# Kernel tuning notes

Hardware: AMD Instinct MI355X
Metric: run time of the kernel (lower is better)

## Reference

```python
import jax, jax.numpy as jnp
import numpy as np

B, K, D = 8, 1024, 512
H, DQ, DV = 8, 64, 64


def setup_inputs() -> dict:
    key = jax.random.key(0)
    ks = jax.random.split(key, 11)
    s = 0.02  # param init scale
    return {
        "query": jax.random.normal(ks[0], (B, K, D), jnp.float32),
        "key": jax.random.normal(ks[1], (B, K, D), jnp.float32),
        "value": jax.random.normal(ks[2], (B, K, D), jnp.float32),
        "Wq": jax.random.normal(ks[3], (D, H * DQ), jnp.float32) * s,
        "bq": jax.random.normal(ks[4], (H * DQ,), jnp.float32) * s,
        "Wk": jax.random.normal(ks[5], (D, H * DQ), jnp.float32) * s,
        "bk": jax.random.normal(ks[6], (H * DQ,), jnp.float32) * s,
        "Wv": jax.random.normal(ks[7], (D, H * DV), jnp.float32) * s,
        "bv": jax.random.normal(ks[8], (H * DV,), jnp.float32) * s,
        "Wo": jax.random.normal(ks[9], (H * DV, D), jnp.float32) * s,
        "bo": jax.random.normal(ks[10], (D,), jnp.float32) * s,
    }


def reference(query, key, value, Wq, bq, Wk, bk, Wv, bv, Wo, bo):
    b, k, _ = query.shape
    # Linear projections, split into heads: chunk(h, dim=-1) + cat(dim=0)
    # is equivalent to reshape (b, k, h, d) with head on a separate axis.
    q = (query @ Wq + bq).reshape(b, k, H, DQ)  # b k h dq
    kk = (key @ Wk + bk).reshape(b, k, H, DQ)   # b k h dq
    v = (value @ Wv + bv).reshape(b, k, H, DV)  # b k h dv
    # NOTE: original scales by sqrt(K) (sequence length), not sqrt(dq).
    scale = 1.0 / jnp.sqrt(jnp.asarray(k, q.dtype))
    scores = jnp.einsum("bqhd,bkhd->bhqk", q, kk) * scale
    attn = jax.nn.softmax(scores, axis=-1)
    ctx = jnp.einsum("bhqk,bkhd->bqhd", attn, v).reshape(b, k, H * DV)
    return ctx @ Wo + bo
```

## Files before the change

kernel.cpp:

```cpp
#include <hip/hip_runtime.h>
#include <hip/hip_bf16.h>

#define DEVI __device__ __forceinline__

typedef __attribute__((ext_vector_type(4))) float f32x4;
typedef __attribute__((ext_vector_type(8))) short bf16x8;

static constexpr int BB  = 8;
static constexpr int SEQ = 1024;
static constexpr int DIM = 512;
static constexpr int NH  = 8;
static constexpr int HD  = 64;
static constexpr int M   = BB * SEQ;


DEVI unsigned short f2bf(float x) {
  unsigned int u = __builtin_bit_cast(unsigned int, x);
  u += 0x7fffu + ((u >> 16) & 1u);
  return (unsigned short)(u >> 16);
}

DEVI float fexp2(float x) {
#if __has_builtin(__builtin_amdgcn_exp2f)
  return __builtin_amdgcn_exp2f(x);
#else
  float r; asm("v_exp_f32 %0, %1" : "=v"(r) : "v"(x)); return r;
#endif
}

DEVI void gload_lds16(const unsigned short* g, unsigned short* l) {
  __builtin_amdgcn_global_load_lds(
      (const __attribute__((address_space(1))) void*)g,
      (__attribute__((address_space(3))) void*)l, 16, 0, 0);
}


__global__ __launch_bounds__(256) void cvt3_kernel(const float* __restrict__ a,
                                                   const float* __restrict__ b,
                                                   const float* __restrict__ c,
                                                   unsigned short* __restrict__ oa,
                                                   unsigned short* __restrict__ ob,
                                                   unsigned short* __restrict__ oc) {
  const float* in = (blockIdx.y == 0) ? a : ((blockIdx.y == 1) ? b : c);
  unsigned short* out = (blockIdx.y == 0) ? oa : ((blockIdx.y == 1) ? ob : oc);
  int i = (blockIdx.x * 256 + threadIdx.x) * 4;
  float4 v = *reinterpret_cast<const float4*>(in + i);
  ushort4 o;
  o.x = f2bf(v.x); o.y = f2bf(v.y); o.z = f2bf(v.z); o.w = f2bf(v.w);
  *reinterpret_cast<ushort4*>(out + i) = o;
}


__global__ __launch_bounds__(256) void cvt_t4_kernel(const float* __restrict__ w0,
                                                     const float* __restrict__ w1,
                                                     const float* __restrict__ w2,
                                                     const float* __restrict__ w3,
                                                     unsigned short* __restrict__ o0,
                                                     unsigned short* __restrict__ o1,
                                                     unsigned short* __restrict__ o2,
                                                     unsigned short* __restrict__ o3) {
  const float* in = (blockIdx.z == 0) ? w0 : ((blockIdx.z == 1) ? w1 : ((blockIdx.z == 2) ? w2 : w3));
  unsigned short* out = (blockIdx.z == 0) ? o0 : ((blockIdx.z == 1) ? o1 : ((blockIdx.z == 2) ? o2 : o3));
  __shared__ float tile[32][33];
  int n0 = blockIdx.x * 32, k0 = blockIdx.y * 32;
  int tx = threadIdx.x & 31, ty = threadIdx.x >> 5;
#pragma unroll
  for (int r = 0; r < 32; r += 8)
    tile[ty + r][tx] = in[(size_t)(k0 + ty + r) * DIM + n0 + tx];
  __syncthreads();
#pragma unroll
  for (int r = 0; r < 32; r += 8)
    out[(size_t)(n0 + ty + r) * DIM + k0 + tx] = f2bf(tile[tx][ty + r]);
}


__global__ __launch_bounds__(256) void gemm_proj(const unsigned short* __restrict__ Aq,
                                                 const unsigned short* __restrict__ Ak,
                                                 const unsigned short* __restrict__ Av,
                                                 const unsigned short* __restrict__ WqT,
                                                 const unsigned short* __restrict__ WkT,
                                                 const unsigned short* __restrict__ WvT,
                                                 const float* __restrict__ bq,
                                                 const float* __restrict__ bk,
                                                 const float* __restrict__ bv,
                                                 unsigned short* __restrict__ qb,
                                                 unsigned short* __restrict__ kb,
                                                 unsigned short* __restrict__ vT,
                                                 float qscale) {
  __shared__ unsigned short smem[24576];
  unsigned short* lA = smem;
  unsigned short* lB = smem + 12288;

  const int z = blockIdx.z;
  const unsigned short* A = (z == 0) ? Aq : ((z == 1) ? Ak : Av);
  const unsigned short* Bt = (z == 0) ? WqT : ((z == 1) ? WkT : WvT);
  const float* bias = (z == 0) ? bq : ((z == 1) ? bk : bv);
  const float gs = (z == 0) ? qscale : 1.0f;

  const int tid = threadIdx.x;
  const int lane = tid & 63, wave = tid >> 6;
  const int wr = wave >> 1, wc = wave & 1;
  const int row0 = blockIdx.x * 128, col0 = blockIdx.y * 128;
  const int lr = lane & 15, lg = lane >> 4;

  f32x4 acc[4][4] = {};

  const int s0a = wave * 64;
  const int sA = s0a + lane, rA = sA >> 2, koA = (sA & 3) * 8;
  const int s0b = 256 + wave * 64;
  const int sB = s0b + lane, rB = sB >> 2, koB = (sB & 3) * 8;

#define GEMM_STAGE(buf, k0)                                                              \
  do {                                                                                   \
    gload_lds16(A + (size_t)(row0 + rA) * DIM + (k0) + koA, &lA[(buf)*4096 + s0a * 8]);  \
    gload_lds16(Bt + (size_t)(col0 + rA) * DIM + (k0) + koA, &lB[(buf)*4096 + s0a * 8]); \
    gload_lds16(A + (size_t)(row0 + rB) * DIM + (k0) + koB, &lA[(buf)*4096 + s0b * 8]);  \
    gload_lds16(Bt + (size_t)(col0 + rB) * DIM + (k0) + koB, &lB[(buf)*4096 + s0b * 8]); \
  } while (0)

#define GEMM_STEP(cur, VMC)                                                              \
  do {                                                                                   \
    asm volatile("s_waitcnt vmcnt(" #VMC ")" ::: "memory");                              \
    __builtin_amdgcn_s_barrier();                                                        \
    bf16x8 af[4], bfr[4];                                                                \
    _Pragma("unroll")                                                                    \
    for (int m = 0; m < 4; ++m)                                                          \
      af[m] = *reinterpret_cast<const bf16x8*>(&lA[(cur)*4096 + (wr * 64 + m * 16 + lr) * 32 + lg * 8]); \
    _Pragma("unroll")                                                                    \
    for (int n = 0; n < 4; ++n)                                                          \
      bfr[n] = *reinterpret_cast<const bf16x8*>(&lB[(cur)*4096 + (wc * 64 + n * 16 + lr) * 32 + lg * 8]); \
    __builtin_amdgcn_s_setprio(1);                                                       \
    _Pragma("unroll")                                                                    \
    for (int m = 0; m < 4; ++m)                                                          \
      _Pragma("unroll")                                                                  \
      for (int n = 0; n < 4; ++n)                                                        \
        acc[m][n] = __builtin_amdgcn_mfma_f32_16x16x32_bf16(af[m], bfr[n], acc[m][n], 0, 0, 0); \
    __builtin_amdgcn_s_setprio(0);                                                       \
    asm volatile("" ::: "memory");                                                       \
    __builtin_amdgcn_s_barrier();                                                        \
  } while (0)

  constexpr int NT = DIM / 32;
  GEMM_STAGE(0, 0);
  GEMM_STAGE(1, 32);
  for (int t = 0; t < NT - 2; ++t) {
    GEMM_STAGE((t + 2) % 3, (t + 2) * 32);
    GEMM_STEP(t % 3, 8);
  }
  GEMM_STEP((NT - 2) % 3, 4);
  GEMM_STEP((NT - 1) % 3, 0);
#undef GEMM_STAGE
#undef GEMM_STEP

  if (z < 2) {
    unsigned short* C = (z == 0) ? qb : kb;
#pragma unroll
    for (int m = 0; m < 4; ++m) {
#pragma unroll
      for (int n = 0; n < 4; ++n) {
        int col = col0 + wc * 64 + n * 16 + lr;
        int r0 = row0 + wr * 64 + m * 16 + lg * 4;
        float bvv = bias[col];
#pragma unroll
        for (int j = 0; j < 4; ++j)
          C[(size_t)(r0 + j) * DIM + col] = f2bf((acc[m][n][j] + bvv) * gs);
      }
    }
  } else {
    unsigned short* ldsT = smem;
    __syncthreads();
#pragma unroll
    for (int m = 0; m < 4; ++m) {
#pragma unroll
      for (int n = 0; n < 4; ++n) {
        const int col = wc * 64 + n * 16 + lr;
        const int r0l = wr * 64 + m * 16 + lg * 4;
        const float bvv = bias[col0 + col];
        ushort4 pk;
        pk.x = f2bf(acc[m][n][0] + bvv);
        pk.y = f2bf(acc[m][n][1] + bvv);
        pk.z = f2bf(acc[m][n][2] + bvv);
        pk.w = f2bf(acc[m][n][3] + bvv);
        *reinterpret_cast<ushort4*>(&ldsT[col * 136 + r0l]) = pk;
      }
    }
    __syncthreads();
    const int b = row0 >> 10, s_loc0 = row0 & 1023;
#pragma unroll
    for (int it = 0; it < 8; ++it) {
      int idx = it * 256 + tid;
      int c = idx >> 4, s8 = idx & 15;
      bf16x8 v = *reinterpret_cast<const bf16x8*>(&ldsT[c * 136 + s8 * 8]);
      *reinterpret_cast<bf16x8*>(
          vT + ((size_t)(b * DIM) + col0 + c) * SEQ + s_loc0 + s8 * 8) = v;
    }
  }
}


__global__ __launch_bounds__(256) void gemm_out(const unsigned short* __restrict__ A,
                                                const unsigned short* __restrict__ Bt,
                                                const float* __restrict__ bias,
                                                float* __restrict__ C) {
  __shared__ unsigned short lA[3][128 * 32];
  __shared__ unsigned short lB[3][128 * 32];
  const int tid = threadIdx.x;
  const int lane = tid & 63, wave = tid >> 6;
  const int wr = wave >> 1, wc = wave & 1;
  const int row0 = blockIdx.x * 128, col0 = blockIdx.y * 128;
  const int lr = lane & 15, lg = lane >> 4;

  f32x4 acc[4][4] = {};

  const int s0a = wave * 64;
  const int sA = s0a + lane, rA = sA >> 2, koA = (sA & 3) * 8;
  const int s0b = 256 + wave * 64;
  const int sB = s0b + lane, rB = sB >> 2, koB = (sB & 3) * 8;

#define GEMM_STAGE(buf, k0)                                                        \
  do {                                                                             \
    gload_lds16(A + (size_t)(row0 + rA) * DIM + (k0) + koA, &lA[buf][s0a * 8]);    \
    gload_lds16(Bt + (size_t)(col0 + rA) * DIM + (k0) + koA, &lB[buf][s0a * 8]);   \
    gload_lds16(A + (size_t)(row0 + rB) * DIM + (k0) + koB, &lA[buf][s0b * 8]);    \
    gload_lds16(Bt + (size_t)(col0 + rB) * DIM + (k0) + koB, &lB[buf][s0b * 8]);   \
  } while (0)

#define GEMM_STEP(cur, VMC)                                                        \
  do {                                                                             \
    asm volatile("s_waitcnt vmcnt(" #VMC ")" ::: "memory");                        \
    __builtin_amdgcn_s_barrier();                                                  \
    bf16x8 af[4], bfr[4];                                                          \
    _Pragma("unroll")                                                              \
    for (int m = 0; m < 4; ++m)                                                    \
      af[m] = *reinterpret_cast<const bf16x8*>(&lA[cur][(wr * 64 + m * 16 + lr) * 32 + lg * 8]); \
    _Pragma("unroll")                                                              \
    for (int n = 0; n < 4; ++n)                                                    \
      bfr[n] = *reinterpret_cast<const bf16x8*>(&lB[cur][(wc * 64 + n * 16 + lr) * 32 + lg * 8]); \
    __builtin_amdgcn_s_setprio(1);                                                 \
    _Pragma("unroll")                                                              \
    for (int m = 0; m < 4; ++m)                                                    \
      _Pragma("unroll")                                                            \
      for (int n = 0; n < 4; ++n)                                                  \
        acc[m][n] = __builtin_amdgcn_mfma_f32_16x16x32_bf16(af[m], bfr[n], acc[m][n], 0, 0, 0); \
    __builtin_amdgcn_s_setprio(0);                                                 \
    asm volatile("" ::: "memory");                                                 \
    __builtin_amdgcn_s_barrier();                                                  \
  } while (0)

  constexpr int NT = DIM / 32;
  GEMM_STAGE(0, 0);
  GEMM_STAGE(1, 32);
  for (int t = 0; t < NT - 2; ++t) {
    GEMM_STAGE((t + 2) % 3, (t + 2) * 32);
    GEMM_STEP((t % 3), 8);
  }
  GEMM_STEP(((NT - 2) % 3), 4);
  GEMM_STEP(((NT - 1) % 3), 0);
#undef GEMM_STAGE
#undef GEMM_STEP

#pragma unroll
  for (int m = 0; m < 4; ++m) {
#pragma unroll
    for (int n = 0; n < 4; ++n) {
      int col = col0 + wc * 64 + n * 16 + lr;
      int r0 = row0 + wr * 64 + m * 16 + lg * 4;
      float bv = bias[col];
#pragma unroll
      for (int j = 0; j < 4; ++j)
        C[(size_t)(r0 + j) * DIM + col] = acc[m][n][j] + bv;
    }
  }
}


__global__ __launch_bounds__(512) void attn_kernel(const unsigned short* __restrict__ qb,
                                                   const unsigned short* __restrict__ kb,
                                                   const unsigned short* __restrict__ vT,
                                                   unsigned short* __restrict__ ctx) {
  __shared__ unsigned short lK[2][64 * 64];
  __shared__ unsigned short lV[2][64 * 64];
  __shared__ unsigned short Pl[8][16 * 72];

  const int b = blockIdx.z, h = blockIdx.y;
  const int tid = threadIdx.x, lane = tid & 63, wave = tid >> 6;
  const int lr = lane & 15, lg = lane >> 4;
  const int q0 = blockIdx.x * 128 + wave * 16;

  const int sr = tid >> 3, sc = (tid & 7) ^ (sr & 7);
  const unsigned short* Kbase = kb + ((size_t)b * SEQ) * DIM + (size_t)h * HD;
  const unsigned short* Vbase = vT + (size_t)(b * NH + h) * HD * SEQ;

  bf16x8 qf0, qf1;
  {
    const unsigned short* qrow = qb + ((size_t)(b * SEQ) + q0 + lr) * DIM + h * HD;
    qf0 = *reinterpret_cast<const bf16x8*>(qrow + lg * 8);
    qf1 = *reinterpret_cast<const bf16x8*>(qrow + 32 + lg * 8);
  }

  float l_r[4] = {0.f, 0.f, 0.f, 0.f};
  f32x4 o_acc[4];
#pragma unroll
  for (int n = 0; n < 4; ++n) o_acc[n] = f32x4{0.f, 0.f, 0.f, 0.f};

  unsigned short* pw = Pl[wave];

#define ATT_STAGE(buf, nk)                                                          \
  do {                                                                              \
    gload_lds16(Kbase + (size_t)((nk) + sr) * DIM + sc * 8, &lK[buf][(wave * 64) * 8]); \
    gload_lds16(Vbase + (size_t)sr * SEQ + (nk) + sc * 8, &lV[buf][(wave * 64) * 8]);   \
  } while (0)

#define ATT_COMPUTE(cur)                                                            \
  do {                                                                              \
    f32x4 st[4];                                                                    \
    __builtin_amdgcn_s_setprio(1);                                                  \
    _Pragma("unroll")                                                               \
    for (int kt = 0; kt < 4; ++kt) {                                                \
      const int row = kt * 16 + lr;                                                 \
      const char* rbase = (const char*)&lK[cur][0] + row * 128;                     \
      const int sw = (row & 7) << 4;                                                \
      bf16x8 kf0 = *reinterpret_cast<const bf16x8*>(rbase + ((lg * 16) ^ sw));      \
      bf16x8 kf1 = *reinterpret_cast<const bf16x8*>(rbase + ((64 + lg * 16) ^ sw)); \
      f32x4 a = {};                                                                 \
      a = __builtin_amdgcn_mfma_f32_16x16x32_bf16(qf0, kf0, a, 0, 0, 0);            \
      a = __builtin_amdgcn_mfma_f32_16x16x32_bf16(qf1, kf1, a, 0, 0, 0);            \
      st[kt] = a;                                                                   \
    }                                                                               \
    __builtin_amdgcn_s_setprio(0);                                                  \
    _Pragma("unroll")                                                               \
    for (int j = 0; j < 4; ++j) {                                                   \
      float p0 = fexp2(st[0][j]);                                                   \
      float p1 = fexp2(st[1][j]);                                                   \
      float p2 = fexp2(st[2][j]);                                                   \
      float p3 = fexp2(st[3][j]);                                                   \
      l_r[j] += (p0 + p1) + (p2 + p3);                                              \
      const int qrow = (lg * 4 + j) * 72;                                           \
      pw[qrow + lr] = f2bf(p0);                                                     \
      pw[qrow + 16 + lr] = f2bf(p1);                                                \
      pw[qrow + 32 + lr] = f2bf(p2);                                                \
      pw[qrow + 48 + lr] = f2bf(p3);                                                \
    }                                                                               \
    _Pragma("unroll")                                                               \
    for (int c = 0; c < 2; ++c) {                                                   \
      bf16x8 pf = *reinterpret_cast<const bf16x8*>((const char*)pw + lr * 144 + c * 64 + lg * 16); \
      __builtin_amdgcn_s_setprio(1);                                                \
      _Pragma("unroll")                                                             \
      for (int n = 0; n < 4; ++n) {                                                 \
        const int row = n * 16 + lr;                                                \
        bf16x8 vf = *reinterpret_cast<const bf16x8*>(                               \
            (const char*)&lV[cur][0] + row * 128 + ((c * 64 + lg * 16) ^ ((row & 7) << 4))); \
        o_acc[n] = __builtin_amdgcn_mfma_f32_16x16x32_bf16(pf, vf, o_acc[n], 0, 0, 0); \
      }                                                                             \
      __builtin_amdgcn_s_setprio(0);                                                \
    }                                                                               \
  } while (0)

  constexpr int NTT = SEQ / 64;
  ATT_STAGE(0, 0);
  for (int t = 0; t < NTT - 1; ++t) {
    const int cur = t & 1;
    ATT_STAGE(cur ^ 1, (t + 1) * 64);
    asm volatile("s_waitcnt vmcnt(2)" ::: "memory");
    __builtin_amdgcn_s_barrier();
    ATT_COMPUTE(cur);
    asm volatile("" ::: "memory");
    __builtin_amdgcn_s_barrier();
  }
  asm volatile("s_waitcnt vmcnt(0)" ::: "memory");
  __builtin_amdgcn_s_barrier();
  ATT_COMPUTE((NTT - 1) & 1);
#undef ATT_STAGE
#undef ATT_COMPUTE

  float invl[4];
#pragma unroll
  for (int j = 0; j < 4; ++j) {
    float l = l_r[j];
#pragma unroll
    for (int msk = 1; msk < 16; msk <<= 1) l += __shfl_xor(l, msk);
    invl[j] = 1.f / l;
  }
#pragma unroll
  for (int n = 0; n < 4; ++n)
#pragma unroll
    for (int j = 0; j < 4; ++j)
      pw[(lg * 4 + j) * 72 + n * 16 + lr] = f2bf(o_acc[n][j] * invl[j]);

#pragma unroll
  for (int it = 0; it < 2; ++it) {
    int idx = it * 64 + lane;
    int r = idx >> 3, cc = idx & 7;
    bf16x8 v = *reinterpret_cast<const bf16x8*>((const char*)pw + r * 144 + cc * 16);
    *reinterpret_cast<bf16x8*>(ctx + ((size_t)(b * SEQ) + q0 + r) * DIM + h * HD + cc * 8) = v;
  }
}


extern "C" void kernel_launch(void* const* d_in, const int* in_sizes, int n_in,
                              void* d_out, int out_size, void* d_ws, size_t ws_size,
                              hipStream_t stream) {
  const float* query = (const float*)d_in[0];
  const float* key_  = (const float*)d_in[1];
  const float* value = (const float*)d_in[2];
  const float* Wq = (const float*)d_in[3];
  const float* bq = (const float*)d_in[4];
  const float* Wk = (const float*)d_in[5];
  const float* bk = (const float*)d_in[6];
  const float* Wv = (const float*)d_in[7];
  const float* bv = (const float*)d_in[8];
  const float* Wo = (const float*)d_in[9];
  const float* bo = (const float*)d_in[10];
  float* out = (float*)d_out;

  unsigned short* ws = (unsigned short*)d_ws;
  const size_t NM = (size_t)M * DIM;
  const size_t NW = (size_t)DIM * DIM;
  unsigned short* xq   = ws;
  unsigned short* xk   = xq + NM;
  unsigned short* xv   = xk + NM;
  unsigned short* qb   = xv + NM;
  unsigned short* kbuf = qb + NM;
  unsigned short* vTb  = kbuf + NM;
  unsigned short* ctx  = vTb + NM;
  unsigned short* Wqt  = ctx + NM;
  unsigned short* Wkt  = Wqt + NW;
  unsigned short* Wvt  = Wkt + NW;
  unsigned short* Wot  = Wvt + NW;

  cvt3_kernel<<<dim3((int)(NM / 1024), 3), 256, 0, stream>>>(query, key_, value, xq, xk, xv);
  cvt_t4_kernel<<<dim3(16, 16, 4), 256, 0, stream>>>(Wq, Wk, Wv, Wo, Wqt, Wkt, Wvt, Wot);

  const float qscale = 0.03125f * 1.4426950408889634f;
  gemm_proj<<<dim3(M / 128, DIM / 128, 3), 256, 0, stream>>>(
      xq, xk, xv, Wqt, Wkt, Wvt, bq, bk, bv, qb, kbuf, vTb, qscale);

  attn_kernel<<<dim3(SEQ / 128, NH, BB), 512, 0, stream>>>(qb, kbuf, vTb, ctx);

  gemm_out<<<dim3(M / 128, DIM / 128), 256, 0, stream>>>(ctx, Wot, bo, out);
}
```

Baseline: 81.41 us.

## Fuse fp32-to-bf16 activation conversion into projection GEMM loads

```diff
diff --git a/kernel.cpp b/kernel.cpp
--- a/kernel.cpp
+++ b/kernel.cpp
@@ -34,20 +34,25 @@
       (__attribute__((address_space(3))) void*)l, 16, 0, 0);
 }
 
-
-__global__ __launch_bounds__(256) void cvt3_kernel(const float* __restrict__ a,
-                                                   const float* __restrict__ b,
-                                                   const float* __restrict__ c,
-                                                   unsigned short* __restrict__ oa,
-                                                   unsigned short* __restrict__ ob,
-                                                   unsigned short* __restrict__ oc) {
-  const float* in = (blockIdx.y == 0) ? a : ((blockIdx.y == 1) ? b : c);
-  unsigned short* out = (blockIdx.y == 0) ? oa : ((blockIdx.y == 1) ? ob : oc);
-  int i = (blockIdx.x * 256 + threadIdx.x) * 4;
-  float4 v = *reinterpret_cast<const float4*>(in + i);
-  ushort4 o;
-  o.x = f2bf(v.x); o.y = f2bf(v.y); o.z = f2bf(v.z); o.w = f2bf(v.w);
-  *reinterpret_cast<ushort4*>(out + i) = o;
+DEVI void gload_lds16f(const float* g, float* l) {
+  __builtin_amdgcn_global_load_lds(
+      (const __attribute__((address_space(1))) void*)g,
+      (__attribute__((address_space(3))) void*)l, 16, 0, 0);
+}
+
+DEVI unsigned int cvtpk(float lo, float hi) {
+  unsigned int r;
+  asm("v_cvt_pk_bf16_f32 %0, %1, %2" : "=v"(r) : "v"(lo), "v"(hi));
+  return r;
+}
+
+DEVI bf16x8 cvt8pk(float4 a, float4 b) {
+  union { unsigned int u[4]; bf16x8 v; } r;
+  r.u[0] = cvtpk(a.x, a.y);
+  r.u[1] = cvtpk(a.z, a.w);
+  r.u[2] = cvtpk(b.x, b.y);
+  r.u[3] = cvtpk(b.z, b.w);
+  return r.v;
 }
 
 
@@ -74,9 +79,9 @@
 }
 
 
-__global__ __launch_bounds__(256) void gemm_proj(const unsigned short* __restrict__ Aq,
-                                                 const unsigned short* __restrict__ Ak,
-                                                 const unsigned short* __restrict__ Av,
+__global__ __launch_bounds__(256) void gemm_proj(const float* __restrict__ Aq,
+                                                 const float* __restrict__ Ak,
+                                                 const float* __restrict__ Av,
                                                  const unsigned short* __restrict__ WqT,
                                                  const unsigned short* __restrict__ WkT,
                                                  const unsigned short* __restrict__ WvT,
@@ -87,12 +92,12 @@
                                                  unsigned short* __restrict__ kb,
                                                  unsigned short* __restrict__ vT,
                                                  float qscale) {
-  __shared__ unsigned short smem[24576];
-  unsigned short* lA = smem;
-  unsigned short* lB = smem + 12288;
+  __shared__ __align__(16) char smem[49152];
+  float* lAf = (float*)smem;
+  unsigned short* lB = (unsigned short*)(smem + 32768);
 
   const int z = blockIdx.z;
-  const unsigned short* A = (z == 0) ? Aq : ((z == 1) ? Ak : Av);
+  const float* A32 = (z == 0) ? Aq : ((z == 1) ? Ak : Av);
   const unsigned short* Bt = (z == 0) ? WqT : ((z == 1) ? WkT : WvT);
   const float* bias = (z == 0) ? bq : ((z == 1) ? bk : bv);
   const float gs = (z == 0) ? qscale : 1.0f;
@@ -105,27 +110,42 @@
 
   f32x4 acc[4][4] = {};
 
+  int arow[4], acsrc[4];
+#pragma unroll
+  for (int it = 0; it < 4; ++it) {
+    int cidx = wave * 256 + it * 64 + lane;
+    arow[it] = cidx >> 3;
+    acsrc[it] = (cidx & 7) ^ (arow[it] & 7);
+  }
   const int s0a = wave * 64;
   const int sA = s0a + lane, rA = sA >> 2, koA = (sA & 3) * 8;
   const int s0b = 256 + wave * 64;
   const int sB = s0b + lane, rB = sB >> 2, koB = (sB & 3) * 8;
 
-#define GEMM_STAGE(buf, k0)                                                              \
+#define PROJ_STAGE(buf, k0)                                                              \
   do {                                                                                   \
-    gload_lds16(A + (size_t)(row0 + rA) * DIM + (k0) + koA, &lA[(buf)*4096 + s0a * 8]);  \
+    _Pragma("unroll")                                                                    \
+    for (int it = 0; it < 4; ++it)                                                       \
+      gload_lds16f(A32 + (size_t)(row0 + arow[it]) * DIM + (k0) + acsrc[it] * 4,         \
+                   &lAf[(buf)*4096 + (wave * 256 + it * 64) * 4]);                       \
     gload_lds16(Bt + (size_t)(col0 + rA) * DIM + (k0) + koA, &lB[(buf)*4096 + s0a * 8]); \
-    gload_lds16(A + (size_t)(row0 + rB) * DIM + (k0) + koB, &lA[(buf)*4096 + s0b * 8]);  \
     gload_lds16(Bt + (size_t)(col0 + rB) * DIM + (k0) + koB, &lB[(buf)*4096 + s0b * 8]); \
   } while (0)
 
-#define GEMM_STEP(cur, VMC)                                                              \
+#define PROJ_STEP(cur, VMC)                                                              \
   do {                                                                                   \
     asm volatile("s_waitcnt vmcnt(" #VMC ")" ::: "memory");                              \
     __builtin_amdgcn_s_barrier();                                                        \
     bf16x8 af[4], bfr[4];                                                                \
     _Pragma("unroll")                                                                    \
-    for (int m = 0; m < 4; ++m)                                                          \
-      af[m] = *reinterpret_cast<const bf16x8*>(&lA[(cur)*4096 + (wr * 64 + m * 16 + lr) * 32 + lg * 8]); \
+    for (int m = 0; m < 4; ++m) {                                                        \
+      const int row = wr * 64 + m * 16 + lr;                                             \
+      const char* aRow = (const char*)&lAf[(cur)*4096] + row * 128;                      \
+      const int swz = (row & 7) << 4;                                                    \
+      float4 f0 = *reinterpret_cast<const float4*>(aRow + ((lg * 32) ^ swz));            \
+      float4 f1 = *reinterpret_cast<const float4*>(aRow + ((lg * 32 + 16) ^ swz));       \
+      af[m] = cvt8pk(f0, f1);                                                            \
+    }                                                                                    \
     _Pragma("unroll")                                                                    \
     for (int n = 0; n < 4; ++n)                                                          \
       bfr[n] = *reinterpret_cast<const bf16x8*>(&lB[(cur)*4096 + (wc * 64 + n * 16 + lr) * 32 + lg * 8]); \
@@ -141,16 +161,14 @@
   } while (0)
 
   constexpr int NT = DIM / 32;
-  GEMM_STAGE(0, 0);
-  GEMM_STAGE(1, 32);
-  for (int t = 0; t < NT - 2; ++t) {
-    GEMM_STAGE((t + 2) % 3, (t + 2) * 32);
-    GEMM_STEP(t % 3, 8);
-  }
-  GEMM_STEP((NT - 2) % 3, 4);
-  GEMM_STEP((NT - 1) % 3, 0);
-#undef GEMM_STAGE
-#undef GEMM_STEP
+  PROJ_STAGE(0, 0);
+  for (int t = 0; t < NT - 1; ++t) {
+    PROJ_STAGE((t + 1) & 1, (t + 1) * 32);
+    PROJ_STEP(t & 1, 6);
+  }
+  PROJ_STEP((NT - 1) & 1, 0);
+#undef PROJ_STAGE
+#undef PROJ_STEP
 
   if (z < 2) {
     unsigned short* C = (z == 0) ? qb : kb;
@@ -167,7 +185,7 @@
       }
     }
   } else {
-    unsigned short* ldsT = smem;
+    unsigned short* ldsT = (unsigned short*)smem;
     __syncthreads();
 #pragma unroll
     for (int m = 0; m < 4; ++m) {
@@ -416,10 +434,7 @@
   unsigned short* ws = (unsigned short*)d_ws;
   const size_t NM = (size_t)M * DIM;
   const size_t NW = (size_t)DIM * DIM;
-  unsigned short* xq   = ws;
-  unsigned short* xk   = xq + NM;
-  unsigned short* xv   = xk + NM;
-  unsigned short* qb   = xv + NM;
+  unsigned short* qb   = ws;
   unsigned short* kbuf = qb + NM;
   unsigned short* vTb  = kbuf + NM;
   unsigned short* ctx  = vTb + NM;
@@ -428,12 +443,11 @@
   unsigned short* Wvt  = Wkt + NW;
   unsigned short* Wot  = Wvt + NW;
 
-  cvt3_kernel<<<dim3((int)(NM / 1024), 3), 256, 0, stream>>>(query, key_, value, xq, xk, xv);
   cvt_t4_kernel<<<dim3(16, 16, 4), 256, 0, stream>>>(Wq, Wk, Wv, Wo, Wqt, Wkt, Wvt, Wot);
 
   const float qscale = 0.03125f * 1.4426950408889634f;
   gemm_proj<<<dim3(M / 128, DIM / 128, 3), 256, 0, stream>>>(
-      xq, xk, xv, Wqt, Wkt, Wvt, bq, bk, bv, qb, kbuf, vTb, qscale);
+      query, key_, value, Wqt, Wkt, Wvt, bq, bk, bv, qb, kbuf, vTb, qscale);
 
   attn_kernel<<<dim3(SEQ / 128, NH, BB), 512, 0, stream>>>(qb, kbuf, vTb, ctx);
 
```

New measurement: 87.73 us. 7.8% more time.
